# Kernel tuning notes

Measured on AMD Instinct MI355X. Metric: run time of the kernel, lower is better.

Reference implementation:

```python
import jax, jax.numpy as jnp
import numpy as np

HEADS, DIM_HEAD = 8, 64
EPS = 1e-5  # torch InstanceNorm1d default


def instance_norm(t):
    # torch InstanceNorm1d(dim_head) applied to (b*h, n, d) normalizes over the
    # last dim d for each (b, h, n); affine=False, biased variance.
    mu = jnp.mean(t, axis=-1, keepdims=True)
    var = jnp.mean((t - mu) ** 2, axis=-1, keepdims=True)
    return (t - mu) * jax.lax.rsqrt(var + EPS)


def setup_inputs() -> dict:
    key = jax.random.key(0)
    k1, k2, k3, k4 = jax.random.split(key, 4)
    B, N, D = 8, 8192, 256
    inner = HEADS * DIM_HEAD  # 512
    x = jax.random.normal(k1, (B, N, D), jnp.float32)
    w_qkv = jax.random.normal(k2, (3 * inner, D), jnp.float32) / np.sqrt(D).astype(np.float32)
    w_out = jax.random.normal(k3, (D, inner), jnp.float32) / np.sqrt(inner).astype(np.float32)
    b_out = 0.01 * jax.random.normal(k4, (D,), jnp.float32)
    return {"x": x, "w_qkv": w_qkv, "w_out": w_out, "b_out": b_out}


def reference(x, w_qkv, w_out, b_out):
    B, N, _ = x.shape
    H, Dh = HEADS, DIM_HEAD
    # fused qkv projection: [B,N,3*H*Dh]
    qkv = jnp.einsum('bnd,ed->bne', x, w_qkv)
    q, k, v = jnp.split(qkv, 3, axis=-1)

    def to_heads(t):
        return t.reshape(B, N, H, Dh).transpose(0, 2, 1, 3)  # b h n d

    q, k, v = to_heads(q), to_heads(k), to_heads(v)
    # galerkin: instance-norm K and V
    k = instance_norm(k)
    v = instance_norm(v)
    # linear (non-softmax) attention: (K^T V) then Q @ (K^T V), scaled by 1/N
    dots = jnp.einsum('bhnd,bhne->bhde', k, v)            # [B,H,Dh,Dh]
    out = jnp.einsum('bhnd,bhde->bhne', q, dots) / N      # [B,H,N,Dh]
    out = out.transpose(0, 2, 1, 3).reshape(B, N, H * Dh)
    return jnp.einsum('bne,de->bnd', out, w_out) + b_out
```

## Files before the change

kernel.cpp:

```cpp
#include <hip/hip_runtime.h>
#include <hip/hip_bf16.h>
#include <stdint.h>

typedef __attribute__((ext_vector_type(8))) __bf16 bf16x8;
typedef __attribute__((ext_vector_type(8))) unsigned short ushort8_t;
typedef __attribute__((ext_vector_type(4))) unsigned short ushort4_t;
typedef __attribute__((ext_vector_type(4))) float f32x4;

#define MFMA16(a, b, c) __builtin_amdgcn_mfma_f32_16x16x32_bf16((a), (b), (c), 0, 0, 0)

static __device__ __forceinline__ unsigned short f2bf(float f) {
  union { float f; unsigned u; } v; v.f = f;
  unsigned r = v.u + 0x7fffu + ((v.u >> 16) & 1u);
  return (unsigned short)(r >> 16);
}
static __device__ __forceinline__ float bf2f(unsigned short u) {
  union { unsigned u; float f; } v; v.u = ((unsigned)u) << 16; return v.f;
}

static __device__ __forceinline__ void gld_lds16(const void* g, void* l) {
  __builtin_amdgcn_global_load_lds((const __attribute__((address_space(1))) void*)g,
                                   (__attribute__((address_space(3))) void*)l, 16, 0, 0);
}

__global__ __launch_bounds__(256) void k_conv(const float* __restrict__ x,
                                              const float* __restrict__ wqkv,
                                              const float* __restrict__ wout,
                                              unsigned short* __restrict__ xb,
                                              unsigned short* __restrict__ wqb,
                                              unsigned short* __restrict__ woutb) {
  const size_t NX = 4194304;
  const size_t NW = 98304;
  const size_t NO = 32768;
  const size_t stride = (size_t)gridDim.x * 256;
  for (size_t i4 = (size_t)blockIdx.x * 256 + threadIdx.x; i4 < NX + NW + NO; i4 += stride) {
    const float* src; unsigned short* dst; size_t off;
    if (i4 < NX)           { src = x;    dst = xb;    off = i4; }
    else if (i4 < NX + NW) { src = wqkv; dst = wqb;   off = i4 - NX; }
    else                   { src = wout; dst = woutb; off = i4 - NX - NW; }
    float4 v = ((const float4*)src)[off];
    ushort4_t o = { f2bf(v.x), f2bf(v.y), f2bf(v.z), f2bf(v.w) };
    *(ushort4_t*)(dst + off * 4) = o;
  }
}

__global__ __launch_bounds__(512) void k_fused(const unsigned short* __restrict__ xb,
                                               const unsigned short* __restrict__ wqb,
                                               float* __restrict__ partials) {
  __shared__ __align__(16) char smem[65536];
  unsigned short* As = (unsigned short*)smem;
  unsigned short* Bs = (unsigned short*)(smem + 32768);
  unsigned short* ovl = (unsigned short*)(smem + 32768);

  const int t = threadIdx.x;
  const int w = t >> 6, lane = t & 63, lr = lane & 15, lg = lane >> 4;
  const int wr = w >> 1, wc = w & 1;
  const int dblk = w >> 1, ep = w & 1;

  const int id = blockIdx.x;
  const int nid = (id & 7) * 128 + (id >> 3);
  const int mg = nid >> 3, h = nid & 7;

  const int srl = lane >> 3, sc = lane & 7;
  const int swz = (sc ^ srl) << 3;

  const unsigned short* bptr[2];
  int aoff[2];
#pragma unroll
  for (int i = 0; i < 2; ++i) {
    const int br = (w * 2 + i) * 8 + srl;
    const int grow = (br < 64) ? (512 + h * 64 + br) : (1024 + h * 64 + (br - 64));
    bptr[i] = wqb + (size_t)grow * 256 + swz;
    aoff[i] = br * 256 + swz;
  }

  f32x4 acc2[2] = {f32x4{0.f, 0.f, 0.f, 0.f}, f32x4{0.f, 0.f, 0.f, 0.f}};

  {
    const unsigned short* am0 = xb + ((size_t)mg * 4 * 128) * 256;
#pragma unroll
    for (int i = 0; i < 2; ++i) {
      gld_lds16(am0 + aoff[i], &As[(w * 2 + i) * 512]);
      gld_lds16(bptr[i],       &Bs[(w * 2 + i) * 512]);
    }
  }

  for (int mi = 0; mi < 4; ++mi) {
    const unsigned short* am = xb + ((size_t)(mg * 4 + mi) * 128) * 256;
    __syncthreads();

    f32x4 acc[2][4];
#pragma unroll
    for (int mb = 0; mb < 2; ++mb)
#pragma unroll
      for (int nb = 0; nb < 4; ++nb) acc[mb][nb] = f32x4{0.f, 0.f, 0.f, 0.f};

    for (int ktt = 0; ktt < 4; ++ktt) {
      const int cur = ktt & 1, nxt = cur ^ 1;
      if (ktt < 3) {
        const int k0 = (ktt + 1) * 64;
#pragma unroll
        for (int i = 0; i < 2; ++i) {
          gld_lds16(am + aoff[i] + k0, &As[nxt * 8192 + (w * 2 + i) * 512]);
          gld_lds16(bptr[i] + k0,      &Bs[nxt * 8192 + (w * 2 + i) * 512]);
        }
      }
      bf16x8 a[2][2], b[4][2];
#pragma unroll
      for (int mb = 0; mb < 2; ++mb) {
        const int R = wr * 32 + mb * 16 + lr;
#pragma unroll
        for (int kh = 0; kh < 2; ++kh)
          a[mb][kh] = *(const bf16x8*)&As[cur * 8192 + R * 64 + ((((kh << 2) + lg) ^ (R & 7)) << 3)];
      }
#pragma unroll
      for (int nb = 0; nb < 4; ++nb) {
        const int E = wc * 64 + nb * 16 + lr;
#pragma unroll
        for (int kh = 0; kh < 2; ++kh)
          b[nb][kh] = *(const bf16x8*)&Bs[cur * 8192 + E * 64 + ((((kh << 2) + lg) ^ (E & 7)) << 3)];
      }
#pragma unroll
      for (int mb = 0; mb < 2; ++mb)
#pragma unroll
        for (int nb = 0; nb < 4; ++nb)
#pragma unroll
          for (int kh = 0; kh < 2; ++kh)
            acc[mb][nb] = MFMA16(a[mb][kh], b[nb][kh], acc[mb][nb]);
      __syncthreads();
    }

    unsigned short* dst = ovl + wc * 8192;
#pragma unroll
    for (int mb = 0; mb < 2; ++mb) {
#pragma unroll
      for (int rg = 0; rg < 4; ++rg) {
        float s1 = acc[mb][0][rg] + acc[mb][1][rg] + acc[mb][2][rg] + acc[mb][3][rg];
        float s2 = acc[mb][0][rg] * acc[mb][0][rg] + acc[mb][1][rg] * acc[mb][1][rg] +
                   acc[mb][2][rg] * acc[mb][2][rg] + acc[mb][3][rg] * acc[mb][3][rg];
        s1 += __shfl_xor(s1, 1); s2 += __shfl_xor(s2, 1);
        s1 += __shfl_xor(s1, 2); s2 += __shfl_xor(s2, 2);
        s1 += __shfl_xor(s1, 4); s2 += __shfl_xor(s2, 4);
        s1 += __shfl_xor(s1, 8); s2 += __shfl_xor(s2, 8);
        const float mean = s1 * (1.f / 64.f);
        const float rs = rsqrtf(s2 * (1.f / 64.f) - mean * mean + 1e-5f);
        const int n = wr * 32 + mb * 16 + lg * 4 + rg;
        const int cn = n >> 6, nn = n & 63;
        const int cc = nn >> 3, cj = nn & 7;
#pragma unroll
        for (int nb = 0; nb < 4; ++nb) {
          const int d = nb * 16 + lr;
          dst[cn * 4096 + d * 64 + ((cc ^ (d & 7)) << 3) + cj] =
              f2bf((acc[mb][nb][rg] - mean) * rs);
        }
      }
    }
    __syncthreads();

    if (mi < 3) {
      const unsigned short* amn = am + 128 * 256;
#pragma unroll
      for (int i = 0; i < 2; ++i)
        gld_lds16(amn + aoff[i], &As[(w * 2 + i) * 512]);
    }

#pragma unroll
    for (int cn = 0; cn < 2; ++cn) {
#pragma unroll
      for (int ns = 0; ns < 64; ns += 32) {
        const int cA = (ns >> 3) + lg;
        const int dd = dblk * 16 + lr;
        bf16x8 af = *(const bf16x8*)&ovl[cn * 4096 + dd * 64 + ((cA ^ (dd & 7)) << 3)];
#pragma unroll
        for (int e = 0; e < 2; ++e) {
          const int ee = (ep * 2 + e) * 16 + lr;
          bf16x8 bv = *(const bf16x8*)&ovl[8192 + cn * 4096 + ee * 64 + ((cA ^ (ee & 7)) << 3)];
          acc2[e] = MFMA16(af, bv, acc2[e]);
        }
      }
    }
    __syncthreads();

    if (mi < 3) {
#pragma unroll
      for (int i = 0; i < 2; ++i)
        gld_lds16(bptr[i], &Bs[(w * 2 + i) * 512]);
    }
  }

  float* pb = partials + ((size_t)mg * 8 + h) * 4096;
#pragma unroll
  for (int e = 0; e < 2; ++e)
#pragma unroll
    for (int rg = 0; rg < 4; ++rg) {
      const int d = dblk * 16 + lg * 4 + rg;
      const int eo = (ep * 2 + e) * 16 + lr;
      pb[d * 64 + eo] = acc2[e][rg];
    }
}

__global__ __launch_bounds__(256) void k_mmat(const float* __restrict__ partials,
                                              const float* __restrict__ wqkv,
                                              unsigned short* __restrict__ tmpT) {
  __shared__ float dl[4096];
  __shared__ float wqls[64 * 256];
  const int bh = blockIdx.x, b = bh >> 3, h = bh & 7;
  const int t = threadIdx.x;
#pragma unroll
  for (int i = 0; i < 4; ++i) {
    int off = t * 16 + i * 4;
    f32x4 s = {0.f, 0.f, 0.f, 0.f};
    for (int c = 0; c < 16; ++c) {
      const size_t chunk = (size_t)(b * 16 + c) * 8 + h;
      f32x4 p = *(const f32x4*)(partials + chunk * 4096 + off);
      s += p;
    }
    *(f32x4*)&dl[off] = s;
  }
#pragma unroll
  for (int i = 0; i < 16; ++i) {
    int idx4 = i * 256 + t;
    int d = idx4 >> 6, c4 = idx4 & 63;
    *(f32x4*)&wqls[d * 256 + c4 * 4] =
        *(const f32x4*)(wqkv + (size_t)(h * 64 + d) * 256 + c4 * 4);
  }
  __syncthreads();
  const int k = t;
  const float scale = 1.0f / 8192.0f;
  float res[64];
  for (int e = 0; e < 64; ++e) {
    float s = 0.f;
#pragma unroll
    for (int d = 0; d < 64; ++d) s += dl[d * 64 + e] * wqls[d * 256 + k];
    res[e] = s * scale;
  }
  unsigned short* dstp = tmpT + (size_t)b * 131072 + (size_t)k * 512 + h * 64;
#pragma unroll
  for (int e8 = 0; e8 < 8; ++e8) {
    ushort8_t o;
#pragma unroll
    for (int j = 0; j < 8; ++j) o[j] = f2bf(res[e8 * 8 + j]);
    *(ushort8_t*)(dstp + e8 * 8) = o;
  }
}

__global__ __launch_bounds__(256) void k_pmat(const unsigned short* __restrict__ woutb,
                                              const unsigned short* __restrict__ tmpT,
                                              unsigned short* __restrict__ pswz) {
  const int bid = blockIdx.x;
  const int b = bid >> 2, oq = (bid >> 1) & 1, kq = bid & 1;
  const int t = threadIdx.x, w = t >> 6, lane = t & 63, lr = lane & 15, lg = lane >> 4;
  const int wr = w >> 1, wc = w & 1;
  const int ob = oq * 128 + wr * 64, kb = kq * 128 + wc * 64;
  const unsigned short* tb = tmpT + (size_t)b * 131072;

  f32x4 acc[4][4];
#pragma unroll
  for (int mb = 0; mb < 4; ++mb)
#pragma unroll
    for (int nb = 0; nb < 4; ++nb) acc[mb][nb] = f32x4{0.f, 0.f, 0.f, 0.f};

  for (int ks = 0; ks < 16; ++ks) {
    bf16x8 a[4], bb[4];
#pragma unroll
    for (int mb = 0; mb < 4; ++mb)
      a[mb] = *(const bf16x8*)(woutb + (size_t)(ob + mb * 16 + lr) * 512 + ks * 32 + lg * 8);
#pragma unroll
    for (int nb = 0; nb < 4; ++nb)
      bb[nb] = *(const bf16x8*)(tb + (size_t)(kb + nb * 16 + lr) * 512 + ks * 32 + lg * 8);
#pragma unroll
    for (int mb = 0; mb < 4; ++mb)
#pragma unroll
      for (int nb = 0; nb < 4; ++nb) acc[mb][nb] = MFMA16(a[mb], bb[nb], acc[mb][nb]);
  }

  unsigned short* pb = pswz + (size_t)b * 65536;
#pragma unroll
  for (int mb = 0; mb < 4; ++mb)
#pragma unroll
    for (int nb = 0; nb < 4; ++nb)
#pragma unroll
      for (int rg = 0; rg < 4; ++rg) {
        int o = ob + mb * 16 + lg * 4 + rg;
        int k = kb + nb * 16 + lr;
        pb[(((k >> 5) * 16 + (o >> 4)) * 64 + (o & 15) + ((k >> 3) & 3) * 16) * 8 + (k & 7)] =
            f2bf(acc[mb][nb][rg]);
      }
}

__global__ __launch_bounds__(512) void k_gemm2(const unsigned short* __restrict__ xb,
                                               const unsigned short* __restrict__ pswz,
                                               const float* __restrict__ bout,
                                               float* __restrict__ out) {
  __shared__ unsigned short As[2][128 * 64];
  const int b = blockIdx.x >> 6, mt = blockIdx.x & 63;
  const long m0 = (long)mt * 128;
  const int t = threadIdx.x, w = t >> 6, lane = t & 63, lr = lane & 15, lg = lane >> 4;
  const int wr = w >> 2, wc = w & 3;
  const unsigned short* qb = xb + ((size_t)b * 8192 + m0) * 256;
  const unsigned short* Mb = pswz + (size_t)b * 65536;
  const int srl = lane >> 3, sc = lane & 7;

#pragma unroll
  for (int i = 0; i < 2; ++i) {
    const int row = (i * 8 + w) * 8 + srl;
    gld_lds16(qb + (size_t)row * 256 + ((sc ^ (row & 7)) << 3),
              &As[0][(i * 8 + w) * 512]);
  }
  __syncthreads();

  f32x4 acc[4][4];
#pragma unroll
  for (int mb = 0; mb < 4; ++mb)
#pragma unroll
    for (int nb = 0; nb < 4; ++nb) acc[mb][nb] = f32x4{0.f, 0.f, 0.f, 0.f};

  for (int ks = 0; ks < 4; ++ks) {
    const int cur = ks & 1, nxt = cur ^ 1;
    if (ks < 3) {
      const int k0 = (ks + 1) * 64;
#pragma unroll
      for (int i = 0; i < 2; ++i) {
        const int row = (i * 8 + w) * 8 + srl;
        gld_lds16(qb + (size_t)row * 256 + k0 + ((sc ^ (row & 7)) << 3),
                  &As[nxt][(i * 8 + w) * 512]);
      }
    }
    bf16x8 a[4][2], bfr[2][4];
#pragma unroll
    for (int mb = 0; mb < 4; ++mb) {
      const int R = wr * 64 + mb * 16 + lr;
#pragma unroll
      for (int kh = 0; kh < 2; ++kh)
        a[mb][kh] = *(const bf16x8*)&As[cur][R * 64 + ((((kh << 2) + lg) ^ (R & 7)) << 3)];
    }
#pragma unroll
    for (int kh = 0; kh < 2; ++kh)
#pragma unroll
      for (int nb = 0; nb < 4; ++nb)
        bfr[kh][nb] = *(const bf16x8*)(Mb + ((((size_t)ks * 2 + kh) * 16 + wc * 4 + nb) * 64 + lane) * 8);
#pragma unroll
    for (int mb = 0; mb < 4; ++mb)
#pragma unroll
      for (int nb = 0; nb < 4; ++nb)
#pragma unroll
        for (int kh = 0; kh < 2; ++kh)
          acc[mb][nb] = MFMA16(a[mb][kh], bfr[kh][nb], acc[mb][nb]);
    __syncthreads();
  }

  float bo[4];
#pragma unroll
  for (int nb = 0; nb < 4; ++nb) bo[nb] = bout[wc * 64 + nb * 16 + lr];
  float* ob = out + ((size_t)b * 8192 + m0) * 256;
#pragma unroll
  for (int mb = 0; mb < 4; ++mb)
#pragma unroll
    for (int nb = 0; nb < 4; ++nb)
#pragma unroll
      for (int rg = 0; rg < 4; ++rg) {
        int row = wr * 64 + mb * 16 + lg * 4 + rg;
        int c = wc * 64 + nb * 16 + lr;
        ob[(size_t)row * 256 + c] = acc[mb][nb][rg] + bo[nb];
      }
}

extern "C" void kernel_launch(void* const* d_in, const int* in_sizes, int n_in,
                              void* d_out, int out_size, void* d_ws, size_t ws_size,
                              hipStream_t stream) {
  const float* x    = (const float*)d_in[0];
  const float* wqkv = (const float*)d_in[1];
  const float* wout = (const float*)d_in[2];
  const float* bout = (const float*)d_in[3];
  float* out = (float*)d_out;

  char* ws = (char*)d_ws;
  unsigned short* xb = (unsigned short*)ws;
  size_t off = (size_t)65536 * 256 * 2;
  unsigned short* wqb = (unsigned short*)(ws + off);
  off += (size_t)1536 * 256 * 2;
  unsigned short* woutb = (unsigned short*)(ws + off);
  off += (size_t)256 * 512 * 2;
  float* partials = (float*)(ws + off);
  off += (size_t)1024 * 4096 * 4;
  unsigned short* tmpT = (unsigned short*)(ws + off);
  off += (size_t)8 * 131072 * 2;
  unsigned short* pswz = (unsigned short*)(ws + off);
  off += (size_t)8 * 65536 * 2;

  k_conv<<<4096, 256, 0, stream>>>(x, wqkv, wout, xb, wqb, woutb);
  k_fused<<<1024, 512, 0, stream>>>(xb, wqb, partials);
  k_mmat<<<64, 256, 0, stream>>>(partials, wqkv, tmpT);
  k_pmat<<<32, 256, 0, stream>>>(woutb, tmpT, pswz);
  k_gemm2<<<512, 512, 0, stream>>>(xb, pswz, bout, out);
}
```

Before: 173.7 us.

## Use padded K/V tiles, drop cross-phase prefetch, stage gemm2 output through LDS

In the fused QKV+norm kernel, the normalized K and V tiles are now written to separate padded LDS buffers (row stride 72) instead of an XOR-swizzled overlay on the B buffer. The early prefetch of the next A/B tile during the K^T V phase is removed, so each m-iteration now starts with a blocking load. In the output GEMM, accumulators are staged through LDS in two halves so the bias add and global stores become coalesced 16-byte float4 writes. The aim is cheaper output stores and simpler LDS indexing, at the cost of losing load/compute overlap in k_fused and adding extra barriers.

```diff
diff --git a/kernel.cpp b/kernel.cpp
--- a/kernel.cpp
+++ b/kernel.cpp
@@ -50,7 +50,8 @@
   __shared__ __align__(16) char smem[65536];
   unsigned short* As = (unsigned short*)smem;
   unsigned short* Bs = (unsigned short*)(smem + 32768);
-  unsigned short* ovl = (unsigned short*)(smem + 32768);
+  unsigned short* kt = (unsigned short*)smem;
+  unsigned short* vt = (unsigned short*)(smem + 18432);
 
   const int t = threadIdx.x;
   const int w = t >> 6, lane = t & 63, lr = lane & 15, lg = lane >> 4;
@@ -76,17 +77,15 @@
 
   f32x4 acc2[2] = {f32x4{0.f, 0.f, 0.f, 0.f}, f32x4{0.f, 0.f, 0.f, 0.f}};
 
-  {
-    const unsigned short* am0 = xb + ((size_t)mg * 4 * 128) * 256;
+  for (int mi = 0; mi < 4; ++mi) {
+    const long m0 = ((long)mg * 4 + mi) * 128;
+    const unsigned short* am = xb + (size_t)m0 * 256;
+
 #pragma unroll
     for (int i = 0; i < 2; ++i) {
-      gld_lds16(am0 + aoff[i], &As[(w * 2 + i) * 512]);
-      gld_lds16(bptr[i],       &Bs[(w * 2 + i) * 512]);
-    }
-  }
-
-  for (int mi = 0; mi < 4; ++mi) {
-    const unsigned short* am = xb + ((size_t)(mg * 4 + mi) * 128) * 256;
+      gld_lds16(am + aoff[i], &As[(w * 2 + i) * 512]);
+      gld_lds16(bptr[i],      &Bs[(w * 2 + i) * 512]);
+    }
     __syncthreads();
 
     f32x4 acc[2][4];
@@ -130,7 +129,7 @@
       __syncthreads();
     }
 
-    unsigned short* dst = ovl + wc * 8192;
+    unsigned short* dst = (wc == 0) ? kt : vt;
 #pragma unroll
     for (int mb = 0; mb < 2; ++mb) {
 #pragma unroll
@@ -146,46 +145,26 @@
         const float rs = rsqrtf(s2 * (1.f / 64.f) - mean * mean + 1e-5f);
         const int n = wr * 32 + mb * 16 + lg * 4 + rg;
         const int cn = n >> 6, nn = n & 63;
-        const int cc = nn >> 3, cj = nn & 7;
-#pragma unroll
-        for (int nb = 0; nb < 4; ++nb) {
-          const int d = nb * 16 + lr;
-          dst[cn * 4096 + d * 64 + ((cc ^ (d & 7)) << 3) + cj] =
-              f2bf((acc[mb][nb][rg] - mean) * rs);
-        }
-      }
-    }
-    __syncthreads();
-
-    if (mi < 3) {
-      const unsigned short* amn = am + 128 * 256;
-#pragma unroll
-      for (int i = 0; i < 2; ++i)
-        gld_lds16(amn + aoff[i], &As[(w * 2 + i) * 512]);
-    }
+#pragma unroll
+        for (int nb = 0; nb < 4; ++nb)
+          dst[cn * 4608 + (nb * 16 + lr) * 72 + nn] = f2bf((acc[mb][nb][rg] - mean) * rs);
+      }
+    }
+    __syncthreads();
 
 #pragma unroll
     for (int cn = 0; cn < 2; ++cn) {
 #pragma unroll
       for (int ns = 0; ns < 64; ns += 32) {
-        const int cA = (ns >> 3) + lg;
-        const int dd = dblk * 16 + lr;
-        bf16x8 af = *(const bf16x8*)&ovl[cn * 4096 + dd * 64 + ((cA ^ (dd & 7)) << 3)];
+        bf16x8 af = *(const bf16x8*)&kt[cn * 4608 + (dblk * 16 + lr) * 72 + ns + lg * 8];
 #pragma unroll
         for (int e = 0; e < 2; ++e) {
-          const int ee = (ep * 2 + e) * 16 + lr;
-          bf16x8 bv = *(const bf16x8*)&ovl[8192 + cn * 4096 + ee * 64 + ((cA ^ (ee & 7)) << 3)];
+          bf16x8 bv = *(const bf16x8*)&vt[cn * 4608 + ((ep * 2 + e) * 16 + lr) * 72 + ns + lg * 8];
           acc2[e] = MFMA16(af, bv, acc2[e]);
         }
       }
     }
     __syncthreads();
-
-    if (mi < 3) {
-#pragma unroll
-      for (int i = 0; i < 2; ++i)
-        gld_lds16(bptr[i], &Bs[(w * 2 + i) * 512]);
-    }
   }
 
   float* pb = partials + ((size_t)mg * 8 + h) * 4096;
@@ -292,7 +271,10 @@
                                                const unsigned short* __restrict__ pswz,
                                                const float* __restrict__ bout,
                                                float* __restrict__ out) {
-  __shared__ unsigned short As[2][128 * 64];
+  __shared__ __align__(16) char smem[65536];
+  unsigned short* As = (unsigned short*)smem;
+  float* lf = (float*)smem;
+
   const int b = blockIdx.x >> 6, mt = blockIdx.x & 63;
   const long m0 = (long)mt * 128;
   const int t = threadIdx.x, w = t >> 6, lane = t & 63, lr = lane & 15, lg = lane >> 4;
@@ -305,7 +287,7 @@
   for (int i = 0; i < 2; ++i) {
     const int row = (i * 8 + w) * 8 + srl;
     gld_lds16(qb + (size_t)row * 256 + ((sc ^ (row & 7)) << 3),
-              &As[0][(i * 8 + w) * 512]);
+              &As[(i * 8 + w) * 512]);
   }
   __syncthreads();
 
@@ -323,7 +305,7 @@
       for (int i = 0; i < 2; ++i) {
         const int row = (i * 8 + w) * 8 + srl;
         gld_lds16(qb + (size_t)row * 256 + k0 + ((sc ^ (row & 7)) << 3),
-                  &As[nxt][(i * 8 + w) * 512]);
+                  &As[nxt * 8192 + (i * 8 + w) * 512]);
       }
     }
     bf16x8 a[4][2], bfr[2][4];
@@ -332,7 +314,7 @@
       const int R = wr * 64 + mb * 16 + lr;
 #pragma unroll
       for (int kh = 0; kh < 2; ++kh)
-        a[mb][kh] = *(const bf16x8*)&As[cur][R * 64 + ((((kh << 2) + lg) ^ (R & 7)) << 3)];
+        a[mb][kh] = *(const bf16x8*)&As[cur * 8192 + R * 64 + ((((kh << 2) + lg) ^ (R & 7)) << 3)];
     }
 #pragma unroll
     for (int kh = 0; kh < 2; ++kh)
@@ -349,20 +331,29 @@
     __syncthreads();
   }
 
-  float bo[4];
-#pragma unroll
-  for (int nb = 0; nb < 4; ++nb) bo[nb] = bout[wc * 64 + nb * 16 + lr];
-  float* ob = out + ((size_t)b * 8192 + m0) * 256;
-#pragma unroll
-  for (int mb = 0; mb < 4; ++mb)
-#pragma unroll
-    for (int nb = 0; nb < 4; ++nb)
-#pragma unroll
-      for (int rg = 0; rg < 4; ++rg) {
-        int row = wr * 64 + mb * 16 + lg * 4 + rg;
-        int c = wc * 64 + nb * 16 + lr;
-        ob[(size_t)row * 256 + c] = acc[mb][nb][rg] + bo[nb];
-      }
+#pragma unroll
+  for (int p = 0; p < 2; ++p) {
+    if (wr == p) {
+#pragma unroll
+      for (int mb = 0; mb < 4; ++mb)
+#pragma unroll
+        for (int nb = 0; nb < 4; ++nb)
+#pragma unroll
+          for (int rg = 0; rg < 4; ++rg)
+            lf[(mb * 16 + lg * 4 + rg) * 256 + wc * 64 + nb * 16 + lr] = acc[mb][nb][rg];
+    }
+    __syncthreads();
+#pragma unroll
+    for (int i = 0; i < 8; ++i) {
+      const int idx = i * 512 + t;
+      const int r = idx >> 6, c4 = idx & 63;
+      f32x4 v = *(f32x4*)&lf[r * 256 + c4 * 4];
+      f32x4 bo4 = *(const f32x4*)(bout + c4 * 4);
+      v += bo4;
+      *(f32x4*)(out + ((size_t)b * 8192 + m0 + p * 64 + r) * 256 + c4 * 4) = v;
+    }
+    __syncthreads();
+  }
 }
 
 extern "C" void kernel_launch(void* const* d_in, const int* in_sizes, int n_in,
```

Result: faster. 164.4 us (-5.4%).
